# Kernel tuning notes

Measured on AMD Instinct MI355X. Metric: run time of the kernel, lower is better.

Reference implementation:

```python
import jax, jax.numpy as jnp
import numpy as np

KERNEL_SIZE = 16
STRIDE = 8
NEG = -1.0e9


def setup_inputs() -> dict:
    key = jax.random.key(0)
    k1, k2, k3, k4, k5 = jax.random.split(key, 5)
    B, C, L = 8, 512, 4096
    x = jax.random.normal(k1, (B, C, L), dtype=jnp.float32)
    mask = jax.random.randint(k2, (B, L), 0, 2).astype(bool)
    W = jax.random.normal(k3, (C, C), dtype=jnp.float32) * 0.02
    b = jax.random.normal(k4, (C,), dtype=jnp.float32) * 0.02
    v = jax.random.normal(k5, (C,), dtype=jnp.float32) * 0.02
    return {"x": x, "mask": mask, "W": W, "b": b, "v": v}


def reference(x, mask, W, b, v):
    # x: [B, C, L], mask: [B, L] (True = masked out)
    B, C, L = x.shape
    win, step = KERNEL_SIZE, STRIDE
    L_pool = 1 + (L - win) // step
    # per-token projection (identical across windows since proj is per-token)
    h = jnp.tanh(jnp.einsum('bcl,dc->bld', x, W) + b)      # [B, L, C]
    s = jnp.einsum('bld,d->bl', h, v)                       # [B, L]
    idx = jnp.arange(L_pool)[:, None] * step + jnp.arange(win)[None, :]
    sw = s[:, idx]
    mw = mask[:, idx]
    sw = jnp.where(mw, NEG, sw)
    w = jax.nn.softmax(sw, axis=-1)
    w = jnp.where(mw, 0.0, w)
    norm = jnp.clip(jnp.sum(w, axis=-1, keepdims=True), 1e-6, None)
    w = w / norm
    xw = x[:, :, idx]
    return jnp.einsum('bcpw,bpw->bcp', xw, w)               # [B, C, L_pool]
```

## Files before the change

kernel.cpp:

```cpp
#include <hip/hip_runtime.h>
#include <hip/hip_bf16.h>
#include <cmath>

#define Bsz 8
#define Csz 512
#define Lsz 4096
#define LPOOL 511
#define NEGV -1000000000.0f

typedef __attribute__((ext_vector_type(8))) short short8;
typedef __attribute__((ext_vector_type(4))) float float4v;

__device__ __forceinline__ float bf2f(short u) {
  unsigned int x = ((unsigned int)(unsigned short)u) << 16;
  return __builtin_bit_cast(float, x);
}

__device__ __forceinline__ float ftanh(float x) {
  float e = __expf(2.0f * x);
  return 1.0f - 2.0f * __builtin_amdgcn_rcpf(e + 1.0f);
}

__global__ __launch_bounds__(256) void prep(const unsigned char* __restrict__ mb,
    int* __restrict__ flag, const float* __restrict__ W,
    __hip_bfloat16* __restrict__ Wts) {
  const int tid = threadIdx.x;
  const int pb = blockIdx.x;
  if (pb == 0) {
    __shared__ int sf;
    if (tid == 0) sf = 0;
    __syncthreads();
    int f = 0;
    for (int i = tid; i < 4096; i += 256)
      if ((i & 3) && mb[i]) f = 1;
    if (f) atomicOr(&sf, 1);
    __syncthreads();
    if (tid == 0) *flag = sf;
  } else {
    int tg = (pb - 1) * 256 + tid;
    int d = tg >> 6, cg = tg & 63;
    float4 w0 = *(const float4*)(W + (size_t)d * 512 + cg * 8);
    float4 w1 = *(const float4*)(W + (size_t)d * 512 + cg * 8 + 4);
    __hip_bfloat16 hb[8];
    hb[0] = __float2bfloat16(w0.x); hb[1] = __float2bfloat16(w0.y);
    hb[2] = __float2bfloat16(w0.z); hb[3] = __float2bfloat16(w0.w);
    hb[4] = __float2bfloat16(w1.x); hb[5] = __float2bfloat16(w1.y);
    hb[6] = __float2bfloat16(w1.z); hb[7] = __float2bfloat16(w1.w);
    int nt = d >> 7, row = d & 127, ks = cg >> 2, seg = cg & 3;
    *(short8*)(Wts + (((size_t)nt * 16 + ks) * 512 + seg * 128 + row) * 8) = *(short8*)hb;
  }
}

__global__ __launch_bounds__(256, 2) void gemm_fused(
    const float* __restrict__ x, const __hip_bfloat16* __restrict__ Wts,
    const float* __restrict__ bias, const float* __restrict__ v,
    float* __restrict__ s) {
  __shared__ short8 sA[4096];
  __shared__ float sXw4[4][672];

  const int tid = threadIdx.x;
  const int lane = tid & 63, wave = tid >> 6;
  const int mt = blockIdx.x;
  const int b = mt >> 6;
  const int l0 = (mt & 63) << 6;

  {
    float* sXw = sXw4[wave];
    const int r = lane >> 1;
    const int q = lane & 1;
    const int ll = lane & 15, ks2 = lane >> 4;
    const float* xg = x + (((size_t)(b * Csz + r)) << 12) + (size_t)(l0 + wave * 16 + q * 8);

    float4 A0a = *(const float4*)(xg);
    float4 A0b = *(const float4*)(xg + 4);
    float4 A1a = *(const float4*)(xg + (1u << 17));
    float4 A1b = *(const float4*)(xg + (1u << 17) + 4);
    float4 A2a = *(const float4*)(xg + (2u << 17));
    float4 A2b = *(const float4*)(xg + (2u << 17) + 4);

    #pragma unroll
    for (int cc = 0; cc < 16; ++cc) {
      float4 Na = A2a, Nb = A2b;
      if (cc < 13) {
        const float* xn = xg + ((size_t)(cc + 3) << 17);
        Na = *(const float4*)(xn);
        Nb = *(const float4*)(xn + 4);
      }
      float* wp = &sXw[r * 21 + q * 8];
      wp[0] = A0a.x; wp[1] = A0a.y; wp[2] = A0a.z; wp[3] = A0a.w;
      wp[4] = A0b.x; wp[5] = A0b.y; wp[6] = A0b.z; wp[7] = A0b.w;
      float tv[8];
      #pragma unroll
      for (int j = 0; j < 8; ++j) tv[j] = sXw[(ks2 * 8 + j) * 21 + ll];
      __hip_bfloat16 ab[8];
      #pragma unroll
      for (int j = 0; j < 8; ++j) ab[j] = __float2bfloat16(tv[j]);
      sA[(cc * 4 + ks2) * 64 + wave * 16 + ll] = *(short8*)ab;
      A0a = A1a; A0b = A1b; A1a = A2a; A1b = A2b; A2a = Na; A2b = Nb;
    }
  }

  const int lr = lane & 15, quad = lane >> 4;
  const int mh = wave >> 1, nh = wave & 1;

  __syncthreads();

  const short8* Bp = (const short8*)Wts + quad * 128 + nh * 64 + lr;
#define LDB(dst, idx)                                                          \
  {                                                                            \
    const short8* bp = Bp + ((size_t)(idx) << 9);                              \
    dst[0] = bp[0]; dst[1] = bp[16]; dst[2] = bp[32]; dst[3] = bp[48];         \
  }
  short8 bA[4], bB[4];
  LDB(bA, 0)

  float sp[2][4];
  #pragma unroll
  for (int mf = 0; mf < 2; ++mf)
    #pragma unroll
    for (int reg = 0; reg < 4; ++reg) sp[mf][reg] = 0.f;

  #pragma unroll
  for (int nt = 0; nt < 4; ++nt) {
    float bl[4], vl[4];
    #pragma unroll
    for (int nf = 0; nf < 4; ++nf) {
      int n = nt * 128 + nh * 64 + nf * 16 + lr;
      bl[nf] = bias[n];
      vl[nf] = v[n];
    }
    float4v acc[2][4];
    #pragma unroll
    for (int mf = 0; mf < 2; ++mf)
      #pragma unroll
      for (int nf = 0; nf < 4; ++nf) acc[mf][nf] = (float4v)0.f;

    #pragma unroll
    for (int k2 = 0; k2 < 8; ++k2) {
      const int ks = k2 * 2;
      const int idx = nt * 16 + ks;
      if (idx + 1 < 64) LDB(bB, idx + 1)
      {
        short8 af[2];
        #pragma unroll
        for (int mf = 0; mf < 2; ++mf)
          af[mf] = sA[(ks * 4 + quad) * 64 + mh * 32 + mf * 16 + lr];
        __builtin_amdgcn_s_setprio(1);
        #pragma unroll
        for (int mf = 0; mf < 2; ++mf)
          #pragma unroll
          for (int nf = 0; nf < 4; ++nf)
            acc[mf][nf] = __builtin_amdgcn_mfma_f32_16x16x32_bf16(
                af[mf], bA[nf], acc[mf][nf], 0, 0, 0);
        __builtin_amdgcn_s_setprio(0);
      }
      if (idx + 2 < 64) LDB(bA, idx + 2)
      {
        short8 af[2];
        #pragma unroll
        for (int mf = 0; mf < 2; ++mf)
          af[mf] = sA[((ks + 1) * 4 + quad) * 64 + mh * 32 + mf * 16 + lr];
        __builtin_amdgcn_s_setprio(1);
        #pragma unroll
        for (int mf = 0; mf < 2; ++mf)
          #pragma unroll
          for (int nf = 0; nf < 4; ++nf)
            acc[mf][nf] = __builtin_amdgcn_mfma_f32_16x16x32_bf16(
                af[mf], bB[nf], acc[mf][nf], 0, 0, 0);
        __builtin_amdgcn_s_setprio(0);
      }
    }
    #pragma unroll
    for (int mf = 0; mf < 2; ++mf)
      #pragma unroll
      for (int reg = 0; reg < 4; ++reg) {
        float pp = 0.f;
        #pragma unroll
        for (int nf = 0; nf < 4; ++nf)
          pp += ftanh(acc[mf][nf][reg] + bl[nf]) * vl[nf];
        sp[mf][reg] += pp;
      }
  }
#undef LDB

  float* sRed = (float*)sXw4;
  float pv[2][4];
  #pragma unroll
  for (int mf = 0; mf < 2; ++mf)
    #pragma unroll
    for (int reg = 0; reg < 4; ++reg) {
      float p = sp[mf][reg];
      p += __shfl_xor(p, 1, 16);
      p += __shfl_xor(p, 2, 16);
      p += __shfl_xor(p, 4, 16);
      p += __shfl_xor(p, 8, 16);
      pv[mf][reg] = p;
    }
  __syncthreads();
  if (nh == 1 && lr == 0) {
    #pragma unroll
    for (int mf = 0; mf < 2; ++mf)
      #pragma unroll
      for (int reg = 0; reg < 4; ++reg)
        sRed[((mh * 2 + mf) * 4 + quad) * 4 + reg] = pv[mf][reg];
  }
  __syncthreads();
  if (nh == 0 && lr == 0) {
    #pragma unroll
    for (int mf = 0; mf < 2; ++mf)
      #pragma unroll
      for (int reg = 0; reg < 4; ++reg)
        s[mt * 64 + mh * 32 + mf * 16 + quad * 4 + reg] =
            pv[mf][reg] + sRed[((mh * 2 + mf) * 4 + quad) * 4 + reg];
  }
}

__global__ __launch_bounds__(256) void pool2(const float* __restrict__ x,
    const float* __restrict__ s, const void* __restrict__ mask,
    const int* __restrict__ flag, float* __restrict__ out) {
  __shared__ float wl[8][17];
  const int t = threadIdx.x;
  const int p0 = blockIdx.x * 8, b = blockIdx.y;
  const int ch = blockIdx.z;
  if (t < 8 && p0 + t < LPOOL) {
    const int p = p0 + t;
    const bool u8 = (*flag != 0);
    const unsigned char* m8 = (const unsigned char*)mask;
    const int* m32 = (const int*)mask;
    const int base = b * Lsz + p * 8;
    float sv[16]; int mv[16];
    float mx = -3.4e38f;
    #pragma unroll
    for (int w = 0; w < 16; ++w) {
      int mk = u8 ? (int)m8[base + w] : m32[base + w];
      float val = mk ? NEGV : s[base + w];
      sv[w] = val; mv[w] = mk;
      mx = fmaxf(mx, val);
    }
    float sum = 0.f;
    #pragma unroll
    for (int w = 0; w < 16; ++w) { sv[w] = expf(sv[w] - mx); sum += sv[w]; }
    float inv = 1.0f / sum;
    float norm = 0.f;
    #pragma unroll
    for (int w = 0; w < 16; ++w) { sv[w] = mv[w] ? 0.f : sv[w] * inv; norm += sv[w]; }
    norm = fmaxf(norm, 1e-6f);
    float rn = 1.0f / norm;
    #pragma unroll
    for (int w = 0; w < 16; ++w) wl[t][w] = sv[w] * rn;
  }
  __syncthreads();
  const int ci = t >> 3, pi = t & 7;
  const int p = p0 + pi;
  if (p >= LPOOL) return;
  float wr[16];
  #pragma unroll
  for (int w = 0; w < 16; ++w) wr[w] = wl[pi][w];
  #pragma unroll
  for (int it = 0; it < 8; ++it) {
    int c = ch * 256 + it * 32 + ci;
    const float* xp = x + ((size_t)b * Csz + c) * Lsz + 8 * p;
    float4 x0 = *(const float4*)(xp);
    float4 x1 = *(const float4*)(xp + 4);
    float4 x2 = *(const float4*)(xp + 8);
    float4 x3 = *(const float4*)(xp + 12);
    float acc = x0.x * wr[0] + x0.y * wr[1] + x0.z * wr[2] + x0.w * wr[3]
              + x1.x * wr[4] + x1.y * wr[5] + x1.z * wr[6] + x1.w * wr[7]
              + x2.x * wr[8] + x2.y * wr[9] + x2.z * wr[10] + x2.w * wr[11]
              + x3.x * wr[12] + x3.y * wr[13] + x3.z * wr[14] + x3.w * wr[15];
    out[((size_t)b * Csz + c) * LPOOL + p] = acc;
  }
}

__global__ void detect_mask(const unsigned char* __restrict__ mb, int* __restrict__ flag) {
  __shared__ int sf;
  int t = threadIdx.x;
  if (t == 0) sf = 0;
  __syncthreads();
  int f = 0;
  for (int i = t; i < 4096; i += 256)
    if ((i & 3) && mb[i]) f = 1;
  if (f) atomicOr(&sf, 1);
  __syncthreads();
  if (t == 0) *flag = sf;
}

__global__ __launch_bounds__(256) void gemm_s_f32(const float* __restrict__ x,
    const float* __restrict__ W, const float* __restrict__ bias,
    const float* __restrict__ v, float* __restrict__ s_out) {
  __shared__ float sA[32][64];
  __shared__ float sB[32][68];
  __shared__ float s_acc[64];
  const int tid = threadIdx.x;
  const int b = blockIdx.y;
  const int l0 = blockIdx.x * 64;
  if (tid < 64) s_acc[tid] = 0.0f;
  const int tx = tid & 15;
  const int ty = tid >> 4;
  const float* xb = x + ((size_t)b * Csz) * Lsz + l0;
  for (int d0 = 0; d0 < Csz; d0 += 64) {
    float acc[4][4] = {{0.f}};
    for (int c0 = 0; c0 < Csz; c0 += 32) {
      __syncthreads();
      #pragma unroll
      for (int it = 0; it < 8; ++it) {
        int idx = tid + it * 256;
        int kc = idx >> 6, ml = idx & 63;
        sA[kc][ml] = xb[(size_t)(c0 + kc) * Lsz + ml];
      }
      #pragma unroll
      for (int it = 0; it < 8; ++it) {
        int idx = tid + it * 256;
        int kc = idx & 31, dj = idx >> 5;
        sB[kc][dj] = W[(size_t)(d0 + dj) * Csz + c0 + kc];
      }
      __syncthreads();
      #pragma unroll
      for (int kc = 0; kc < 32; ++kc) {
        float4 a  = *(const float4*)(&sA[kc][tx << 2]);
        float4 w4 = *(const float4*)(&sB[kc][ty << 2]);
        acc[0][0] += a.x * w4.x; acc[0][1] += a.x * w4.y; acc[0][2] += a.x * w4.z; acc[0][3] += a.x * w4.w;
        acc[1][0] += a.y * w4.x; acc[1][1] += a.y * w4.y; acc[1][2] += a.y * w4.z; acc[1][3] += a.y * w4.w;
        acc[2][0] += a.z * w4.x; acc[2][1] += a.z * w4.y; acc[2][2] += a.z * w4.z; acc[2][3] += a.z * w4.w;
        acc[3][0] += a.w * w4.x; acc[3][1] += a.w * w4.y; acc[3][2] += a.w * w4.z; acc[3][3] += a.w * w4.w;
      }
    }
    float part[4] = {0.f, 0.f, 0.f, 0.f};
    #pragma unroll
    for (int j = 0; j < 4; ++j) {
      int d = d0 + (ty << 2) + j;
      float bj = bias[d], vj = v[d];
      #pragma unroll
      for (int i = 0; i < 4; ++i)
        part[i] += tanhf(acc[i][j] + bj) * vj;
    }
    #pragma unroll
    for (int i = 0; i < 4; ++i)
      atomicAdd(&s_acc[(tx << 2) + i], part[i]);
  }
  __syncthreads();
  if (tid < 64) s_out[(size_t)b * Lsz + l0 + tid] = s_acc[tid];
}

__global__ void win_weights(const float* __restrict__ s, const void* __restrict__ mask,
                            const int* __restrict__ flag, float* __restrict__ wgt) {
  int t = blockIdx.x * blockDim.x + threadIdx.x;
  if (t >= Bsz * LPOOL) return;
  int b = t / LPOOL, p = t - b * LPOOL;
  const bool u8 = (*flag != 0);
  const unsigned char* m8 = (const unsigned char*)mask;
  const int* m32 = (const int*)mask;
  float sv[16]; int mv[16];
  float mx = -3.4e38f;
  int base = b * Lsz + p * 8;
  #pragma unroll
  for (int w = 0; w < 16; ++w) {
    int mk = u8 ? (int)m8[base + w] : m32[base + w];
    float val = mk ? NEGV : s[base + w];
    sv[w] = val; mv[w] = mk;
    mx = fmaxf(mx, val);
  }
  float sum = 0.f;
  #pragma unroll
  for (int w = 0; w < 16; ++w) { sv[w] = expf(sv[w] - mx); sum += sv[w]; }
  float inv = 1.0f / sum;
  float norm = 0.f;
  #pragma unroll
  for (int w = 0; w < 16; ++w) { sv[w] = mv[w] ? 0.f : sv[w] * inv; norm += sv[w]; }
  norm = fmaxf(norm, 1e-6f);
  float rn = 1.0f / norm;
  #pragma unroll
  for (int w = 0; w < 16; ++w) wgt[t * 16 + w] = sv[w] * rn;
}

__global__ __launch_bounds__(256) void pool_out(const float* __restrict__ x,
    const float* __restrict__ wgt, float* __restrict__ out) {
  __shared__ float xrow[Lsz];
  int bc = blockIdx.x;
  int c = bc & (Csz - 1);
  int b = bc >> 9;
  const float* xr = x + ((size_t)b * Csz + c) * Lsz;
  int tid = threadIdx.x;
  #pragma unroll
  for (int it = 0; it < 4; ++it) {
    int idx = (tid + it * 256) << 2;
    *(float4*)(&xrow[idx]) = *(const float4*)(&xr[idx]);
  }
  __syncthreads();
  const float* wb = wgt + (size_t)b * LPOOL * 16;
  float* ob = out + ((size_t)b * Csz + c) * LPOOL;
  for (int p = tid; p < LPOOL; p += 256) {
    const float4* wp = (const float4*)(wb + p * 16);
    const float4* xp = (const float4*)(&xrow[p * 8]);
    float acc = 0.f;
    #pragma unroll
    for (int q = 0; q < 4; ++q) {
      float4 wv = wp[q], xv = xp[q];
      acc += xv.x * wv.x + xv.y * wv.y + xv.z * wv.z + xv.w * wv.w;
    }
    ob[p] = acc;
  }
}

extern "C" void kernel_launch(void* const* d_in, const int* in_sizes, int n_in,
                              void* d_out, int out_size, void* d_ws, size_t ws_size,
                              hipStream_t stream) {
  const float* x    = (const float*)d_in[0];
  const void*  mask = d_in[1];
  const float* W    = (const float*)d_in[2];
  const float* bias = (const float*)d_in[3];
  const float* v    = (const float*)d_in[4];
  float* out = (float*)d_out;

  char* wsb = (char*)d_ws;
  int*   flag = (int*)wsb;
  float* s    = (float*)(wsb + 256);
  float* wgt  = (float*)(wsb + 131328);
  __hip_bfloat16* Wts = (__hip_bfloat16*)(wsb + 393216);
  const size_t NEED = 917504;

  if (ws_size >= NEED) {
    prep<<<129, 256, 0, stream>>>((const unsigned char*)mask, flag, W, Wts);
    gemm_fused<<<512, 256, 0, stream>>>(x, Wts, bias, v, s);
    pool2<<<dim3(64, Bsz, 2), 256, 0, stream>>>(x, s, mask, flag, out);
  } else {
    detect_mask<<<1, 256, 0, stream>>>((const unsigned char*)mask, flag);
    gemm_s_f32<<<dim3(Lsz / 64, Bsz), 256, 0, stream>>>(x, W, bias, v, s);
    win_weights<<<(Bsz * LPOOL + 255) / 256, 256, 0, stream>>>(s, mask, flag, wgt);
    pool_out<<<Bsz * Csz, 256, 0, stream>>>(x, wgt, out);
  }
}
```

Before: 149.4 us.

## Halve GEMM M-tile to 32 rows and remap pool threads to per-channel windows

The fused GEMM now uses 128-thread blocks covering 32 tokens each, launching 1024 blocks instead of 512. The intent is more blocks per CU and better load balance across the many CUs, at the cost of each block reading the full W for fewer rows. The pooling kernel is remapped so each thread handles one channel and 8 consecutive pool outputs. It loads a contiguous 72-float span of x once and reuses the overlapping window elements, rather than reloading 16 floats per output. Weights are read from shared memory as float4, with a guarded tail for the last partial block.

```diff
diff --git a/kernel.cpp b/kernel.cpp
--- a/kernel.cpp
+++ b/kernel.cpp
@@ -51,21 +51,21 @@
   }
 }
 
-__global__ __launch_bounds__(256, 2) void gemm_fused(
+__global__ __launch_bounds__(128, 2) void gemm_fused(
     const float* __restrict__ x, const __hip_bfloat16* __restrict__ Wts,
     const float* __restrict__ bias, const float* __restrict__ v,
     float* __restrict__ s) {
-  __shared__ short8 sA[4096];
-  __shared__ float sXw4[4][672];
+  __shared__ short8 sA[2048];
+  __shared__ float sXw2[2][672];
 
   const int tid = threadIdx.x;
   const int lane = tid & 63, wave = tid >> 6;
   const int mt = blockIdx.x;
-  const int b = mt >> 6;
-  const int l0 = (mt & 63) << 6;
+  const int b = mt >> 7;
+  const int l0 = (mt & 127) << 5;
 
   {
-    float* sXw = sXw4[wave];
+    float* sXw = sXw2[wave];
     const int r = lane >> 1;
     const int q = lane & 1;
     const int ll = lane & 15, ks2 = lane >> 4;
@@ -95,13 +95,13 @@
       __hip_bfloat16 ab[8];
       #pragma unroll
       for (int j = 0; j < 8; ++j) ab[j] = __float2bfloat16(tv[j]);
-      sA[(cc * 4 + ks2) * 64 + wave * 16 + ll] = *(short8*)ab;
+      sA[(cc * 4 + ks2) * 32 + wave * 16 + ll] = *(short8*)ab;
       A0a = A1a; A0b = A1b; A1a = A2a; A1b = A2b; A2a = Na; A2b = Nb;
     }
   }
 
   const int lr = lane & 15, quad = lane >> 4;
-  const int mh = wave >> 1, nh = wave & 1;
+  const int nh = wave;
 
   __syncthreads();
 
@@ -144,7 +144,7 @@
         short8 af[2];
         #pragma unroll
         for (int mf = 0; mf < 2; ++mf)
-          af[mf] = sA[(ks * 4 + quad) * 64 + mh * 32 + mf * 16 + lr];
+          af[mf] = sA[(ks * 4 + quad) * 32 + mf * 16 + lr];
         __builtin_amdgcn_s_setprio(1);
         #pragma unroll
         for (int mf = 0; mf < 2; ++mf)
@@ -159,7 +159,7 @@
         short8 af[2];
         #pragma unroll
         for (int mf = 0; mf < 2; ++mf)
-          af[mf] = sA[((ks + 1) * 4 + quad) * 64 + mh * 32 + mf * 16 + lr];
+          af[mf] = sA[((ks + 1) * 4 + quad) * 32 + mf * 16 + lr];
         __builtin_amdgcn_s_setprio(1);
         #pragma unroll
         for (int mf = 0; mf < 2; ++mf)
@@ -183,7 +183,7 @@
   }
 #undef LDB
 
-  float* sRed = (float*)sXw4;
+  float* sRed = (float*)sXw2;
   float pv[2][4];
   #pragma unroll
   for (int mf = 0; mf < 2; ++mf)
@@ -202,7 +202,7 @@
     for (int mf = 0; mf < 2; ++mf)
       #pragma unroll
       for (int reg = 0; reg < 4; ++reg)
-        sRed[((mh * 2 + mf) * 4 + quad) * 4 + reg] = pv[mf][reg];
+        sRed[mf * 16 + quad * 4 + reg] = pv[mf][reg];
   }
   __syncthreads();
   if (nh == 0 && lr == 0) {
@@ -210,18 +210,18 @@
     for (int mf = 0; mf < 2; ++mf)
       #pragma unroll
       for (int reg = 0; reg < 4; ++reg)
-        s[mt * 64 + mh * 32 + mf * 16 + quad * 4 + reg] =
-            pv[mf][reg] + sRed[((mh * 2 + mf) * 4 + quad) * 4 + reg];
+        s[mt * 32 + mf * 16 + quad * 4 + reg] =
+            pv[mf][reg] + sRed[mf * 16 + quad * 4 + reg];
   }
 }
 
 __global__ __launch_bounds__(256) void pool2(const float* __restrict__ x,
     const float* __restrict__ s, const void* __restrict__ mask,
     const int* __restrict__ flag, float* __restrict__ out) {
-  __shared__ float wl[8][17];
+  __shared__ __align__(16) float wl[8][16];
   const int t = threadIdx.x;
-  const int p0 = blockIdx.x * 8, b = blockIdx.y;
-  const int ch = blockIdx.z;
+  const int bx = blockIdx.x;
+  const int p0 = bx * 8, b = blockIdx.y, ch = blockIdx.z;
   if (t < 8 && p0 + t < LPOOL) {
     const int p = p0 + t;
     const bool u8 = (*flag != 0);
@@ -250,25 +250,38 @@
     for (int w = 0; w < 16; ++w) wl[t][w] = sv[w] * rn;
   }
   __syncthreads();
-  const int ci = t >> 3, pi = t & 7;
-  const int p = p0 + pi;
-  if (p >= LPOOL) return;
-  float wr[16];
-  #pragma unroll
-  for (int w = 0; w < 16; ++w) wr[w] = wl[pi][w];
-  #pragma unroll
-  for (int it = 0; it < 8; ++it) {
-    int c = ch * 256 + it * 32 + ci;
-    const float* xp = x + ((size_t)b * Csz + c) * Lsz + 8 * p;
-    float4 x0 = *(const float4*)(xp);
-    float4 x1 = *(const float4*)(xp + 4);
-    float4 x2 = *(const float4*)(xp + 8);
-    float4 x3 = *(const float4*)(xp + 12);
-    float acc = x0.x * wr[0] + x0.y * wr[1] + x0.z * wr[2] + x0.w * wr[3]
-              + x1.x * wr[4] + x1.y * wr[5] + x1.z * wr[6] + x1.w * wr[7]
-              + x2.x * wr[8] + x2.y * wr[9] + x2.z * wr[10] + x2.w * wr[11]
-              + x3.x * wr[12] + x3.y * wr[13] + x3.z * wr[14] + x3.w * wr[15];
-    out[((size_t)b * Csz + c) * LPOOL + p] = acc;
+  const int c = ch * 256 + t;
+  const float* xp = x + ((size_t)b * Csz + c) * Lsz + p0 * 8;
+  float fb[72];
+  #pragma unroll
+  for (int i = 0; i < 16; ++i) {
+    float4 vv = *(const float4*)(xp + i * 4);
+    fb[i * 4 + 0] = vv.x; fb[i * 4 + 1] = vv.y;
+    fb[i * 4 + 2] = vv.z; fb[i * 4 + 3] = vv.w;
+  }
+  const bool full = (bx < 63);
+  if (full) {
+    float4 v16 = *(const float4*)(xp + 64);
+    float4 v17 = *(const float4*)(xp + 68);
+    fb[64] = v16.x; fb[65] = v16.y; fb[66] = v16.z; fb[67] = v16.w;
+    fb[68] = v17.x; fb[69] = v17.y; fb[70] = v17.z; fb[71] = v17.w;
+  } else {
+    #pragma unroll
+    for (int i = 64; i < 72; ++i) fb[i] = 0.f;
+  }
+  float* ob = out + ((size_t)b * Csz + c) * LPOOL + p0;
+  #pragma unroll
+  for (int j = 0; j < 8; ++j) {
+    if (j == 7 && !full) break;
+    float4 w0 = *(const float4*)(&wl[j][0]);
+    float4 w1 = *(const float4*)(&wl[j][4]);
+    float4 w2 = *(const float4*)(&wl[j][8]);
+    float4 w3 = *(const float4*)(&wl[j][12]);
+    float acc = fb[8*j+0] * w0.x + fb[8*j+1] * w0.y + fb[8*j+2] * w0.z + fb[8*j+3] * w0.w
+              + fb[8*j+4] * w1.x + fb[8*j+5] * w1.y + fb[8*j+6] * w1.z + fb[8*j+7] * w1.w
+              + fb[8*j+8] * w2.x + fb[8*j+9] * w2.y + fb[8*j+10] * w2.z + fb[8*j+11] * w2.w
+              + fb[8*j+12] * w3.x + fb[8*j+13] * w3.y + fb[8*j+14] * w3.z + fb[8*j+15] * w3.w;
+    ob[j] = acc;
   }
 }
 
@@ -421,7 +434,7 @@
 
   if (ws_size >= NEED) {
     prep<<<129, 256, 0, stream>>>((const unsigned char*)mask, flag, W, Wts);
-    gemm_fused<<<512, 256, 0, stream>>>(x, Wts, bias, v, s);
+    gemm_fused<<<1024, 128, 0, stream>>>(x, Wts, bias, v, s);
     pool2<<<dim3(64, Bsz, 2), 256, 0, stream>>>(x, s, mask, flag, out);
   } else {
     detect_mask<<<1, 256, 0, stream>>>((const unsigned char*)mask, flag);
```

Measured after the change: 152.4 us. 1.02x slower.

## Deepen B-fragment prefetch to four stages and split pooling into weights+row kernels

Applied to the files above, without the earlier changes.

The GEMM inner loop now keeps a four-deep ring of W fragments in registers, issuing each load four k-steps ahead instead of double-buffering two ahead. This gives global loads more time to land before the MFMAs need them. The fused pool2 kernel is replaced on the fast path by a separate window-weight kernel plus a per-(batch,channel) pooling kernel that stages a full x row in shared memory for coalesced reads. The cost is one more launch, a round trip of the weights through global memory, and higher register pressure in the GEMM.

```diff
diff --git a/kernel.cpp b/kernel.cpp
--- a/kernel.cpp
+++ b/kernel.cpp
@@ -111,8 +111,8 @@
     const short8* bp = Bp + ((size_t)(idx) << 9);                              \
     dst[0] = bp[0]; dst[1] = bp[16]; dst[2] = bp[32]; dst[3] = bp[48];         \
   }
-  short8 bA[4], bB[4];
-  LDB(bA, 0)
+  short8 bq[4][4];
+  LDB(bq[0], 0) LDB(bq[1], 1) LDB(bq[2], 2) LDB(bq[3], 3)
 
   float sp[2][4];
   #pragma unroll
@@ -136,39 +136,20 @@
       for (int nf = 0; nf < 4; ++nf) acc[mf][nf] = (float4v)0.f;
 
     #pragma unroll
-    for (int k2 = 0; k2 < 8; ++k2) {
-      const int ks = k2 * 2;
+    for (int ks = 0; ks < 16; ++ks) {
       const int idx = nt * 16 + ks;
-      if (idx + 1 < 64) LDB(bB, idx + 1)
-      {
-        short8 af[2];
+      short8 af[2];
+      af[0] = sA[(ks * 4 + quad) * 64 + mh * 32 + lr];
+      af[1] = sA[(ks * 4 + quad) * 64 + mh * 32 + 16 + lr];
+      __builtin_amdgcn_s_setprio(1);
+      #pragma unroll
+      for (int mf = 0; mf < 2; ++mf)
         #pragma unroll
-        for (int mf = 0; mf < 2; ++mf)
-          af[mf] = sA[(ks * 4 + quad) * 64 + mh * 32 + mf * 16 + lr];
-        __builtin_amdgcn_s_setprio(1);
-        #pragma unroll
-        for (int mf = 0; mf < 2; ++mf)
-          #pragma unroll
-          for (int nf = 0; nf < 4; ++nf)
-            acc[mf][nf] = __builtin_amdgcn_mfma_f32_16x16x32_bf16(
-                af[mf], bA[nf], acc[mf][nf], 0, 0, 0);
-        __builtin_amdgcn_s_setprio(0);
-      }
-      if (idx + 2 < 64) LDB(bA, idx + 2)
-      {
-        short8 af[2];
-        #pragma unroll
-        for (int mf = 0; mf < 2; ++mf)
-          af[mf] = sA[((ks + 1) * 4 + quad) * 64 + mh * 32 + mf * 16 + lr];
-        __builtin_amdgcn_s_setprio(1);
-        #pragma unroll
-        for (int mf = 0; mf < 2; ++mf)
-          #pragma unroll
-          for (int nf = 0; nf < 4; ++nf)
-            acc[mf][nf] = __builtin_amdgcn_mfma_f32_16x16x32_bf16(
-                af[mf], bB[nf], acc[mf][nf], 0, 0, 0);
-        __builtin_amdgcn_s_setprio(0);
-      }
+        for (int nf = 0; nf < 4; ++nf)
+          acc[mf][nf] = __builtin_amdgcn_mfma_f32_16x16x32_bf16(
+              af[mf], bq[idx & 3][nf], acc[mf][nf], 0, 0, 0);
+      __builtin_amdgcn_s_setprio(0);
+      if (idx + 4 < 64) LDB(bq[idx & 3], idx + 4)
     }
     #pragma unroll
     for (int mf = 0; mf < 2; ++mf)
@@ -215,60 +196,63 @@
   }
 }
 
-__global__ __launch_bounds__(256) void pool2(const float* __restrict__ x,
-    const float* __restrict__ s, const void* __restrict__ mask,
-    const int* __restrict__ flag, float* __restrict__ out) {
-  __shared__ float wl[8][17];
-  const int t = threadIdx.x;
-  const int p0 = blockIdx.x * 8, b = blockIdx.y;
-  const int ch = blockIdx.z;
-  if (t < 8 && p0 + t < LPOOL) {
-    const int p = p0 + t;
-    const bool u8 = (*flag != 0);
-    const unsigned char* m8 = (const unsigned char*)mask;
-    const int* m32 = (const int*)mask;
-    const int base = b * Lsz + p * 8;
-    float sv[16]; int mv[16];
-    float mx = -3.4e38f;
-    #pragma unroll
-    for (int w = 0; w < 16; ++w) {
-      int mk = u8 ? (int)m8[base + w] : m32[base + w];
-      float val = mk ? NEGV : s[base + w];
-      sv[w] = val; mv[w] = mk;
-      mx = fmaxf(mx, val);
-    }
-    float sum = 0.f;
-    #pragma unroll
-    for (int w = 0; w < 16; ++w) { sv[w] = expf(sv[w] - mx); sum += sv[w]; }
-    float inv = 1.0f / sum;
-    float norm = 0.f;
-    #pragma unroll
-    for (int w = 0; w < 16; ++w) { sv[w] = mv[w] ? 0.f : sv[w] * inv; norm += sv[w]; }
-    norm = fmaxf(norm, 1e-6f);
-    float rn = 1.0f / norm;
-    #pragma unroll
-    for (int w = 0; w < 16; ++w) wl[t][w] = sv[w] * rn;
-  }
-  __syncthreads();
-  const int ci = t >> 3, pi = t & 7;
-  const int p = p0 + pi;
-  if (p >= LPOOL) return;
-  float wr[16];
-  #pragma unroll
-  for (int w = 0; w < 16; ++w) wr[w] = wl[pi][w];
-  #pragma unroll
-  for (int it = 0; it < 8; ++it) {
-    int c = ch * 256 + it * 32 + ci;
-    const float* xp = x + ((size_t)b * Csz + c) * Lsz + 8 * p;
-    float4 x0 = *(const float4*)(xp);
-    float4 x1 = *(const float4*)(xp + 4);
-    float4 x2 = *(const float4*)(xp + 8);
-    float4 x3 = *(const float4*)(xp + 12);
-    float acc = x0.x * wr[0] + x0.y * wr[1] + x0.z * wr[2] + x0.w * wr[3]
-              + x1.x * wr[4] + x1.y * wr[5] + x1.z * wr[6] + x1.w * wr[7]
-              + x2.x * wr[8] + x2.y * wr[9] + x2.z * wr[10] + x2.w * wr[11]
-              + x3.x * wr[12] + x3.y * wr[13] + x3.z * wr[14] + x3.w * wr[15];
-    out[((size_t)b * Csz + c) * LPOOL + p] = acc;
+__global__ void win_weights(const float* __restrict__ s, const void* __restrict__ mask,
+                            const int* __restrict__ flag, float* __restrict__ wgt) {
+  int t = blockIdx.x * blockDim.x + threadIdx.x;
+  if (t >= Bsz * LPOOL) return;
+  int b = t / LPOOL, p = t - b * LPOOL;
+  const bool u8 = (*flag != 0);
+  const unsigned char* m8 = (const unsigned char*)mask;
+  const int* m32 = (const int*)mask;
+  float sv[16]; int mv[16];
+  float mx = -3.4e38f;
+  int base = b * Lsz + p * 8;
+  #pragma unroll
+  for (int w = 0; w < 16; ++w) {
+    int mk = u8 ? (int)m8[base + w] : m32[base + w];
+    float val = mk ? NEGV : s[base + w];
+    sv[w] = val; mv[w] = mk;
+    mx = fmaxf(mx, val);
+  }
+  float sum = 0.f;
+  #pragma unroll
+  for (int w = 0; w < 16; ++w) { sv[w] = expf(sv[w] - mx); sum += sv[w]; }
+  float inv = 1.0f / sum;
+  float norm = 0.f;
+  #pragma unroll
+  for (int w = 0; w < 16; ++w) { sv[w] = mv[w] ? 0.f : sv[w] * inv; norm += sv[w]; }
+  norm = fmaxf(norm, 1e-6f);
+  float rn = 1.0f / norm;
+  #pragma unroll
+  for (int w = 0; w < 16; ++w) wgt[t * 16 + w] = sv[w] * rn;
+}
+
+__global__ __launch_bounds__(256) void pool_out(const float* __restrict__ x,
+    const float* __restrict__ wgt, float* __restrict__ out) {
+  __shared__ float xrow[Lsz];
+  int bc = blockIdx.x;
+  int c = bc & (Csz - 1);
+  int b = bc >> 9;
+  const float* xr = x + ((size_t)b * Csz + c) * Lsz;
+  int tid = threadIdx.x;
+  #pragma unroll
+  for (int it = 0; it < 4; ++it) {
+    int idx = (tid + it * 256) << 2;
+    *(float4*)(&xrow[idx]) = *(const float4*)(&xr[idx]);
+  }
+  __syncthreads();
+  const float* wb = wgt + (size_t)b * LPOOL * 16;
+  float* ob = out + ((size_t)b * Csz + c) * LPOOL;
+  for (int p = tid; p < LPOOL; p += 256) {
+    const float4* wp = (const float4*)(wb + p * 16);
+    const float4* xp = (const float4*)(&xrow[p * 8]);
+    float acc = 0.f;
+    #pragma unroll
+    for (int q = 0; q < 4; ++q) {
+      float4 wv = wp[q], xv = xp[q];
+      acc += xv.x * wv.x + xv.y * wv.y + xv.z * wv.z + xv.w * wv.w;
+    }
+    ob[p] = acc;
   }
 }
 
@@ -342,66 +326,6 @@
   if (tid < 64) s_out[(size_t)b * Lsz + l0 + tid] = s_acc[tid];
 }
 
-__global__ void win_weights(const float* __restrict__ s, const void* __restrict__ mask,
-                            const int* __restrict__ flag, float* __restrict__ wgt) {
-  int t = blockIdx.x * blockDim.x + threadIdx.x;
-  if (t >= Bsz * LPOOL) return;
-  int b = t / LPOOL, p = t - b * LPOOL;
-  const bool u8 = (*flag != 0);
-  const unsigned char* m8 = (const unsigned char*)mask;
-  const int* m32 = (const int*)mask;
-  float sv[16]; int mv[16];
-  float mx = -3.4e38f;
-  int base = b * Lsz + p * 8;
-  #pragma unroll
-  for (int w = 0; w < 16; ++w) {
-    int mk = u8 ? (int)m8[base + w] : m32[base + w];
-    float val = mk ? NEGV : s[base + w];
-    sv[w] = val; mv[w] = mk;
-    mx = fmaxf(mx, val);
-  }
-  float sum = 0.f;
-  #pragma unroll
-  for (int w = 0; w < 16; ++w) { sv[w] = expf(sv[w] - mx); sum += sv[w]; }
-  float inv = 1.0f / sum;
-  float norm = 0.f;
-  #pragma unroll
-  for (int w = 0; w < 16; ++w) { sv[w] = mv[w] ? 0.f : sv[w] * inv; norm += sv[w]; }
-  norm = fmaxf(norm, 1e-6f);
-  float rn = 1.0f / norm;
-  #pragma unroll
-  for (int w = 0; w < 16; ++w) wgt[t * 16 + w] = sv[w] * rn;
-}
-
-__global__ __launch_bounds__(256) void pool_out(const float* __restrict__ x,
-    const float* __restrict__ wgt, float* __restrict__ out) {
-  __shared__ float xrow[Lsz];
-  int bc = blockIdx.x;
-  int c = bc & (Csz - 1);
-  int b = bc >> 9;
-  const float* xr = x + ((size_t)b * Csz + c) * Lsz;
-  int tid = threadIdx.x;
-  #pragma unroll
-  for (int it = 0; it < 4; ++it) {
-    int idx = (tid + it * 256) << 2;
-    *(float4*)(&xrow[idx]) = *(const float4*)(&xr[idx]);
-  }
-  __syncthreads();
-  const float* wb = wgt + (size_t)b * LPOOL * 16;
-  float* ob = out + ((size_t)b * Csz + c) * LPOOL;
-  for (int p = tid; p < LPOOL; p += 256) {
-    const float4* wp = (const float4*)(wb + p * 16);
-    const float4* xp = (const float4*)(&xrow[p * 8]);
-    float acc = 0.f;
-    #pragma unroll
-    for (int q = 0; q < 4; ++q) {
-      float4 wv = wp[q], xv = xp[q];
-      acc += xv.x * wv.x + xv.y * wv.y + xv.z * wv.z + xv.w * wv.w;
-    }
-    ob[p] = acc;
-  }
-}
-
 extern "C" void kernel_launch(void* const* d_in, const int* in_sizes, int n_in,
                               void* d_out, int out_size, void* d_ws, size_t ws_size,
                               hipStream_t stream) {
@@ -422,7 +346,8 @@
   if (ws_size >= NEED) {
     prep<<<129, 256, 0, stream>>>((const unsigned char*)mask, flag, W, Wts);
     gemm_fused<<<512, 256, 0, stream>>>(x, Wts, bias, v, s);
-    pool2<<<dim3(64, Bsz, 2), 256, 0, stream>>>(x, s, mask, flag, out);
+    win_weights<<<(Bsz * LPOOL + 255) / 256, 256, 0, stream>>>(s, mask, flag, wgt);
+    pool_out<<<Bsz * Csz, 256, 0, stream>>>(x, wgt, out);
   } else {
     detect_mask<<<1, 256, 0, stream>>>((const unsigned char*)mask, flag);
     gemm_s_f32<<<dim3(Lsz / 64, Bsz), 256, 0, stream>>>(x, W, bias, v, s);
```

Result: no change. 147.0 us (-1.6%).
